# Kernel optimization log

Measured on AMD Instinct MI355X. Metric: run time of the kernel, lower is better.

The kernel has to match this reference:

```python
import jax, jax.numpy as jnp
import numpy as np

PI = 3.141592653589793


def setup_inputs() -> dict:
    key = jax.random.key(0)
    k1, k2, k3, k4 = jax.random.split(key, 4)
    B, N, C, H, V = 4, 4096, 128, 8, 16
    inputs = jax.random.normal(k1, (B, N, C), dtype=jnp.float32)
    dist = jax.random.uniform(k2, (N, N), dtype=jnp.float32)
    r = jax.random.normal(k3, (H, 1, 1), dtype=jnp.float32)
    weight = jax.random.normal(k4, (H, C, V), dtype=jnp.float32)
    return {"inputs": inputs, "dist": dist, "r": r, "weight": weight, "locality": 64}


def reference(inputs, dist, r, weight, locality):
    # scaled_dist: (H, N, N) -- learnable bandwidth per head via tan/sin transform
    scaled = dist[None, :, :] * jnp.tan(0.25 * PI * (1.0 + jnp.sin(r)))
    # quantile-based local masking along last axis (linear interpolation,
    # matching tfp.stats.percentile with interpolation='linear')
    mask = jnp.percentile(scaled, float(locality), axis=-1, keepdims=True, method="linear")
    fmax = jnp.finfo(jnp.float32).max
    scaled = jnp.where(scaled <= mask, scaled, fmax)
    # softmax over key axis of -scaled_dist (masked entries -> -fmax -> ~0 weight)
    att = jax.nn.softmax(-scaled, axis=-1)  # (H, N, N)
    # per-head value projection: (B,N,C) x (H,C,V) -> (B,H,N,V)
    value = jnp.einsum("bnj,hjk->bhnk", inputs, weight)
    # attention aggregation: (H,N,N) x (B,H,N,V) -> (B,H,N,V)
    concat = jnp.einsum("hnj,bhjd->bhnd", att, value)
    B, H, N, V = concat.shape
    concat = concat.transpose(0, 2, 1, 3).reshape(B, N, H * V)  # (B, N, hid_dim)
    # tf.keras.activations.gelu defaults to exact (non-approximate) gelu
    return jax.nn.gelu(concat, approximate=False)
```

## Files before the change

### kernel.cpp

```cpp
#include <hip/hip_runtime.h>
#include <hip/hip_bf16.h>
#include <math.h>

#define NN 4096
#define NC 128
#define NH 8
#define NV 16
#define NB 4
#define BD 64

typedef _Float16 half8 __attribute__((ext_vector_type(8)));
typedef __fp16  fp16x2 __attribute__((ext_vector_type(2)));
typedef float floatx4 __attribute__((ext_vector_type(4)));

__device__ __forceinline__ int get_loc(const int* locp){
    int lr = locp[0];
    return (lr >= 0 && lr <= 100) ? lr : 64;
}
__device__ __forceinline__ float head_scale(const float* rr, int h){
    float ts = tanf(0.78539816339744831f * (1.0f + sinf(rr[h])));
    if (!(ts > 0.f)) ts = (ts == 0.f) ? 1e-20f : 1e20f;
    if (ts > 1e20f) ts = 1e20f;
    return ts;
}
__device__ __forceinline__ void lds_barrier(){
    __asm__ __volatile__("s_waitcnt lgkmcnt(0)\n\ts_barrier" ::: "memory");
}

__global__ __launch_bounds__(256) void k_rowstats(const float* __restrict__ dist,
                                                  const int* __restrict__ locp,
                                                  float* __restrict__ Kval,
                                                  float* __restrict__ xminp){
    __shared__ unsigned int hist[4][256];
    __shared__ float cand[1024];
    __shared__ unsigned int cnt, selb_s, basec_s, xminu;
    const int i = blockIdx.x, t = threadIdx.x;
    const int wv = t >> 6, lane = t & 63;
    const int loc = get_loc(locp);
    const unsigned int rank = (unsigned int)(((long long)loc * (NN - 1)) / 100) + 1u;

    float v[16];
    const float4* rp = (const float4*)(dist + (size_t)i * NN);
#pragma unroll
    for (int k = 0; k < 4; k++){
        float4 x4 = rp[k * 256 + t];
        v[4*k+0] = x4.x; v[4*k+1] = x4.y; v[4*k+2] = x4.z; v[4*k+3] = x4.w;
    }
    for (int k = t; k < 1024; k += 256) ((unsigned int*)hist)[k] = 0;
    if (t == 0){ cnt = 0; selb_s = 255u; basec_s = 0u; xminu = 0xFFFFFFFFu; }
    __syncthreads();

    float lmin = 1e30f;
#pragma unroll
    for (int u = 0; u < 16; u++){
        float x = v[u];
        lmin = fminf(lmin, x);
        int b = (int)(x * 256.0f); b = b < 0 ? 0 : (b > 255 ? 255 : b);
        atomicAdd(&hist[wv][b], 1u);
    }
#pragma unroll
    for (int off = 1; off < 64; off <<= 1) lmin = fminf(lmin, __shfl_xor(lmin, off));
    if (lane == 0) atomicMin(&xminu, __float_as_uint(lmin));
    __syncthreads();

    if (t < 64){
        unsigned int lp[4];
        unsigned int run = 0;
#pragma unroll
        for (int q = 0; q < 4; q++){
            int b = 4 * t + q;
            run += hist[0][b] + hist[1][b] + hist[2][b] + hist[3][b];
            lp[q] = run;
        }
        unsigned int incl = run;
#pragma unroll
        for (int d = 1; d < 64; d <<= 1){
            unsigned int y = __shfl_up(incl, d);
            if (t >= d) incl += y;
        }
        unsigned int excl = incl - run;
        if (excl < rank && rank <= incl){
#pragma unroll
            for (int q = 0; q < 4; q++){
                if (excl + lp[q] >= rank){
                    selb_s  = (unsigned int)(4 * t + q);
                    basec_s = excl + (q ? lp[q-1] : 0u);
                    break;
                }
            }
        }
    }
    __syncthreads();
    const unsigned int sb = selb_s;
    if (t == 0) Kval[i] = ((float)sb + 1.0f) * 0.00390625f;
#pragma unroll
    for (int u = 0; u < 16; u++){
        float x = v[u];
        int b = (int)(x * 256.0f); b = b < 0 ? 0 : (b > 255 ? 255 : b);
        if ((unsigned int)b == sb){
            unsigned int idx = atomicAdd(&cnt, 1u);
            if (idx < 1024u) cand[idx] = x;
        }
    }
    __syncthreads();
    const unsigned int n = cnt > 1024u ? 1024u : cnt;
    const unsigned int need = rank - basec_s;
    for (unsigned int c0 = t; c0 < n; c0 += 256){
        float x = cand[c0];
        unsigned int lt = 0, le = 0;
        for (unsigned int k2 = 0; k2 < n; k2++){
            float y = cand[k2];
            lt += (y < x); le += (y <= x);
        }
        if (lt < need && need <= le) Kval[i] = x;
    }
    if (t == 0) xminp[i] = __uint_as_float(xminu);
}

__global__ __launch_bounds__(256) void k_value(const float* __restrict__ in,
                                               const float* __restrict__ wgt,
                                               _Float16* __restrict__ val_t){
    __shared__ float insh[NC * 65];
    __shared__ float wsh[NC * NV];
    const int j0 = blockIdx.x * 16;
    const int h  = blockIdx.y;
    const int t  = threadIdx.x;

    for (int k = t; k < NC * NV; k += 256) wsh[k] = wgt[h * NC * NV + k];
#pragma unroll
    for (int k = 0; k < 32; k++){
        int idx = k * 256 + t;
        int p = idx >> 7, c = idx & 127;
        int b = p >> 4, jl = p & 15;
        insh[c * 65 + jl * 4 + b] = in[((size_t)b * NN + j0 + jl) * NC + c];
    }
    __syncthreads();

    const int r = t & 63, dq = t >> 6;
    const int jl = r >> 2, b = r & 3;
    float a0 = 0.f, a1 = 0.f, a2 = 0.f, a3 = 0.f;
#pragma unroll 8
    for (int c = 0; c < NC; c++){
        float x = insh[c * 65 + r];
        float4 w4 = *(const float4*)&wsh[c * NV + dq * 4];
        a0 = fmaf(x, w4.x, a0);
        a1 = fmaf(x, w4.y, a1);
        a2 = fmaf(x, w4.z, a2);
        a3 = fmaf(x, w4.w, a3);
    }
    const size_t base = ((size_t)(h * BD + b * NV + dq * 4)) * NN + j0 + jl;
    val_t[base         ] = (_Float16)a0;
    val_t[base + NN    ] = (_Float16)a1;
    val_t[base + 2 * NN] = (_Float16)a2;
    val_t[base + 3 * NN] = (_Float16)a3;
}

__global__ __launch_bounds__(256) void k_att(const float* __restrict__ dist,
                                             const float* __restrict__ rr,
                                             const _Float16* __restrict__ val_t,
                                             const float* __restrict__ Kvalp,
                                             const float* __restrict__ xminp,
                                             float* __restrict__ out){
    __shared__ alignas(16) _Float16 wtile[2][32 * 72];
    __shared__ alignas(16) _Float16 vtile[2][64 * 72];

    const int l   = blockIdx.x + (NN / 32) * blockIdx.y;
    const int xcd = l & 7;
    const int s   = l >> 3;
    const int i0  = (xcd * 16 + (s >> 3)) * 32;
    const int h   = s & 7;

    const int t = threadIdx.x;
    const int lane = t & 63, wv = t >> 6;
    const float ts  = head_scale(rr, h);
    const float ts2 = ts * 1.44269504088896f;

    const int il = t >> 3, jq = t & 7;
    const int vrow = t >> 3, vpart = t & 7;
    const float kvi  = Kvalp[i0 + il];
    const float txmi = ts2 * xminp[i0 + il];
    const float nts2 = -ts2;

    half8 ones;
#pragma unroll
    for (int u = 0; u < 8; u++) ones[u] = (_Float16)1.0f;

    const float* dp = dist + (size_t)(i0 + il) * NN + jq * 8;
    const _Float16* vp0 = val_t + (size_t)(h * BD + vrow) * NN + vpart * 8;
    const _Float16* vp1 = vp0 + (size_t)32 * NN;

    floatx4 acc0 = (floatx4){0.f,0.f,0.f,0.f};
    floatx4 acc1 = (floatx4){0.f,0.f,0.f,0.f};
    floatx4 accs = (floatx4){0.f,0.f,0.f,0.f};

    const int is16 = (wv & 1) * 16;
    const int bh   = (wv >> 1) * 32;
    const int aoff  = (is16 + (lane & 15)) * 72 + (lane >> 4) * 8;
    const int boff0 = (bh + (lane & 15)) * 72 + (lane >> 4) * 8;
    const int boff1 = boff0 + 16 * 72;
    const int voff0 = vrow * 72 + vpart * 8;
    const int voff1 = (vrow + 32) * 72 + vpart * 8;
    const int woff  = il * 72 + jq * 8;

    uint4  Av0, Av1, Bv0, Bv1;
    float4 Ad0, Ad1, Bd0, Bd1;

#define LOADSET(V0, V1, D0, D1) do{                                          \
        V0 = *(const uint4*)vp0;  vp0 += 64;                                 \
        V1 = *(const uint4*)vp1;  vp1 += 64;                                 \
        D0 = *(const float4*)dp;                                             \
        D1 = *(const float4*)(dp + 4);  dp += 64; }while(0)

#define STAGE(BUF, V0, V1, D0, D1) do{                                       \
        *(uint4*)&vtile[BUF][voff0] = V0;                                    \
        *(uint4*)&vtile[BUF][voff1] = V1;                                    \
        const float dd_[8] = {D0.x,D0.y,D0.z,D0.w,D1.x,D1.y,D1.z,D1.w};      \
        union { half8 h8; fp16x2 h2[4]; } uu_;                               \
        _Pragma("unroll")                                                    \
        for (int u_ = 0; u_ < 4; u_++){                                      \
            float a0_ = fmaf(nts2, dd_[2*u_  ], txmi);                       \
            float a1_ = fmaf(nts2, dd_[2*u_+1], txmi);                       \
            a0_ = (dd_[2*u_  ] <= kvi) ? a0_ : -20000.0f;                    \
            a1_ = (dd_[2*u_+1] <= kvi) ? a1_ : -20000.0f;                    \
            uu_.h2[u_] = __builtin_amdgcn_cvt_pkrtz(                         \
                __builtin_amdgcn_exp2f(a0_), __builtin_amdgcn_exp2f(a1_));   \
        }                                                                    \
        *(half8*)&wtile[BUF][woff] = uu_.h8; }while(0)

#define MFMA_T(BUF) do{                                                      \
        _Pragma("unroll")                                                    \
        for (int kc_ = 0; kc_ < 2; kc_++){                                   \
            half8 af = *(const half8*)&wtile[BUF][aoff  + kc_ * 32];         \
            half8 b0 = *(const half8*)&vtile[BUF][boff0 + kc_ * 32];         \
            half8 b1 = *(const half8*)&vtile[BUF][boff1 + kc_ * 32];         \
            acc0 = __builtin_amdgcn_mfma_f32_16x16x32_f16(af, b0, acc0, 0, 0, 0); \
            acc1 = __builtin_amdgcn_mfma_f32_16x16x32_f16(af, b1, acc1, 0, 0, 0); \
            accs = __builtin_amdgcn_mfma_f32_16x16x32_f16(af, ones, accs, 0, 0, 0); \
        } }while(0)

    LOADSET(Av0, Av1, Ad0, Ad1);
    LOADSET(Bv0, Bv1, Bd0, Bd1);
    STAGE(0, Av0, Av1, Ad0, Ad1);

    for (int jp = 0; jp < 31; jp++){
        LOADSET(Av0, Av1, Ad0, Ad1);
        lds_barrier();
        MFMA_T(0);
        STAGE(1, Bv0, Bv1, Bd0, Bd1);
        LOADSET(Bv0, Bv1, Bd0, Bd1);
        lds_barrier();
        MFMA_T(1);
        STAGE(0, Av0, Av1, Ad0, Ad1);
    }
    lds_barrier();
    MFMA_T(0);
    STAGE(1, Bv0, Bv1, Bd0, Bd1);
    lds_barrier();
    MFMA_T(1);

#undef LOADSET
#undef STAGE
#undef MFMA_T

    const int m0 = (lane >> 4) * 4;
    const int d  = lane & 15;
#pragma unroll
    for (int r4 = 0; r4 < 4; r4++){
        const int iloc = is16 + m0 + r4;
        const float inv_s = 1.0f / fmaxf(accs[r4], 1e-30f);
#pragma unroll
        for (int nt = 0; nt < 2; nt++){
            const int b = (wv >> 1) * 2 + nt;
            float c = acc0[r4], c1 = acc1[r4];
            float cc = (nt == 0 ? c : c1) * inv_s;
            float g = 0.5f * cc * (1.0f + erff(cc * 0.70710678118654752f));
            out[((size_t)b * NN + i0 + iloc) * (NH * NV) + h * NV + d] = g;
        }
    }
}

extern "C" void kernel_launch(void* const* d_in, const int* in_sizes, int n_in,
                              void* d_out, int out_size, void* d_ws, size_t ws_size,
                              hipStream_t stream) {
    const float* in   = (const float*)d_in[0];
    const float* dist = (const float*)d_in[1];
    const float* r    = (const float*)d_in[2];
    const float* wgt  = (const float*)d_in[3];
    const int*   loc  = (const int*)d_in[4];
    float* out = (float*)d_out;

    float* Kval = (float*)d_ws;
    float* xmin = Kval + NN;
    _Float16* val_t = (_Float16*)((char*)d_ws + 2 * (size_t)NN * sizeof(float));

    k_rowstats<<<NN, 256, 0, stream>>>(dist, loc, Kval, xmin);
    k_value<<<dim3(NN / 16, NH), 256, 0, stream>>>(in, wgt, val_t);
    k_att<<<dim3(NN / 32, NH), 256, 0, stream>>>(dist, r, val_t, Kval, xmin, out);
}
```

Before: 177.6 us.

## Compute attention weights in registers and rewrite value projection with split-fp16 MFMA

The attention kernel now gives each wave 16 query rows and computes the softmax weights directly into MFMA A-fragments in registers. This drops the shared-memory weight tile, and each block covers 64 rows against all four batches, so every staged value tile is reused by more rows. The value projection is rewritten as an MFMA GEMM that splits each fp32 input into fp16 hi and lo parts to keep accuracy, replacing the scalar FMA loop. The cost is more registers per thread and a grid of fewer, larger blocks, which may lower occupancy.

```diff
diff --git a/kernel.cpp b/kernel.cpp
--- a/kernel.cpp
+++ b/kernel.cpp
@@ -120,39 +120,70 @@
 __global__ __launch_bounds__(256) void k_value(const float* __restrict__ in,
                                                const float* __restrict__ wgt,
                                                _Float16* __restrict__ val_t){
-    __shared__ float insh[NC * 65];
-    __shared__ float wsh[NC * NV];
-    const int j0 = blockIdx.x * 16;
-    const int h  = blockIdx.y;
-    const int t  = threadIdx.x;
-
-    for (int k = t; k < NC * NV; k += 256) wsh[k] = wgt[h * NC * NV + k];
-#pragma unroll
-    for (int k = 0; k < 32; k++){
-        int idx = k * 256 + t;
-        int p = idx >> 7, c = idx & 127;
-        int b = p >> 4, jl = p & 15;
-        insh[c * 65 + jl * 4 + b] = in[((size_t)b * NN + j0 + jl) * NC + c];
-    }
-    __syncthreads();
-
-    const int r = t & 63, dq = t >> 6;
-    const int jl = r >> 2, b = r & 3;
-    float a0 = 0.f, a1 = 0.f, a2 = 0.f, a3 = 0.f;
-#pragma unroll 8
-    for (int c = 0; c < NC; c++){
-        float x = insh[c * 65 + r];
-        float4 w4 = *(const float4*)&wsh[c * NV + dq * 4];
-        a0 = fmaf(x, w4.x, a0);
-        a1 = fmaf(x, w4.y, a1);
-        a2 = fmaf(x, w4.z, a2);
-        a3 = fmaf(x, w4.w, a3);
-    }
-    const size_t base = ((size_t)(h * BD + b * NV + dq * 4)) * NN + j0 + jl;
-    val_t[base         ] = (_Float16)a0;
-    val_t[base + NN    ] = (_Float16)a1;
-    val_t[base + 2 * NN] = (_Float16)a2;
-    val_t[base + 3 * NN] = (_Float16)a3;
+    __shared__ _Float16 Wt[NH * NV * 136];
+    const int b  = blockIdx.y;
+    const int j0 = blockIdx.x * 32;
+    const int t  = threadIdx.x, lane = t & 63, wv = t >> 6;
+
+    for (int w = t; w < NH * NC * NV; w += 256){
+        int h = w >> 11, c = (w >> 4) & 127, v = w & 15;
+        Wt[(h * 16 + v) * 136 + c] = (_Float16)wgt[w];
+    }
+    __syncthreads();
+
+    const int kl = (lane >> 4) * 8;
+    half8 Bf[2][4];
+#pragma unroll
+    for (int nt = 0; nt < 2; nt++){
+        const int hv = wv * 32 + nt * 16 + (lane & 15);
+#pragma unroll
+        for (int kc = 0; kc < 4; kc++)
+            Bf[nt][kc] = *(const half8*)&Wt[hv * 136 + kc * 32 + kl];
+    }
+
+    floatx4 acc[2][2];
+#pragma unroll
+    for (int a = 0; a < 2; a++)
+#pragma unroll
+        for (int c = 0; c < 2; c++) acc[a][c] = (floatx4){0.f,0.f,0.f,0.f};
+
+    const float* ip = in + ((size_t)b * NN + j0 + (lane & 15)) * NC + kl;
+#pragma unroll
+    for (int jm = 0; jm < 2; jm++){
+        const float* ipm = ip + jm * 16 * NC;
+#pragma unroll
+        for (int kc = 0; kc < 4; kc++){
+            float4 x0 = *(const float4*)(ipm + kc * 32);
+            float4 x1 = *(const float4*)(ipm + kc * 32 + 4);
+            const float xs[8] = {x0.x,x0.y,x0.z,x0.w,x1.x,x1.y,x1.z,x1.w};
+            union { half8 h8; fp16x2 h2[4]; } hi, lo;
+#pragma unroll
+            for (int u = 0; u < 4; u++){
+                hi.h2[u] = __builtin_amdgcn_cvt_pkrtz(xs[2*u], xs[2*u+1]);
+                float r0 = xs[2*u]   - (float)hi.h2[u][0];
+                float r1 = xs[2*u+1] - (float)hi.h2[u][1];
+                lo.h2[u] = __builtin_amdgcn_cvt_pkrtz(r0, r1);
+            }
+#pragma unroll
+            for (int nt = 0; nt < 2; nt++){
+                acc[jm][nt] = __builtin_amdgcn_mfma_f32_16x16x32_f16(hi.h8, Bf[nt][kc], acc[jm][nt], 0, 0, 0);
+                acc[jm][nt] = __builtin_amdgcn_mfma_f32_16x16x32_f16(lo.h8, Bf[nt][kc], acc[jm][nt], 0, 0, 0);
+            }
+        }
+    }
+
+    const int jw = (lane >> 4) * 4;
+#pragma unroll
+    for (int jm = 0; jm < 2; jm++)
+#pragma unroll
+        for (int nt = 0; nt < 2; nt++){
+            const int hv  = wv * 32 + nt * 16 + (lane & 15);
+            const int row = (hv >> 4) * BD + b * NV + (hv & 15);
+            union { _Float16 h[4]; uint2 u; } o;
+#pragma unroll
+            for (int u = 0; u < 4; u++) o.h[u] = (_Float16)acc[jm][nt][u];
+            *(uint2*)&val_t[(size_t)row * NN + j0 + jm * 16 + jw] = o.u;
+        }
 }
 
 __global__ __launch_bounds__(256) void k_att(const float* __restrict__ dist,
@@ -161,120 +192,126 @@
                                              const float* __restrict__ Kvalp,
                                              const float* __restrict__ xminp,
                                              float* __restrict__ out){
-    __shared__ alignas(16) _Float16 wtile[2][32 * 72];
     __shared__ alignas(16) _Float16 vtile[2][64 * 72];
 
-    const int l   = blockIdx.x + (NN / 32) * blockIdx.y;
+    const int l   = blockIdx.x + (NN / 64) * blockIdx.y;
     const int xcd = l & 7;
     const int s   = l >> 3;
-    const int i0  = (xcd * 16 + (s >> 3)) * 32;
+    const int i0  = (xcd * 8 + (s >> 3)) * 64;
     const int h   = s & 7;
 
-    const int t = threadIdx.x;
-    const int lane = t & 63, wv = t >> 6;
-    const float ts  = head_scale(rr, h);
-    const float ts2 = ts * 1.44269504088896f;
-
-    const int il = t >> 3, jq = t & 7;
+    const int t = threadIdx.x, lane = t & 63, wv = t >> 6;
+    const float ts   = head_scale(rr, h);
+    const float ts2  = ts * 1.44269504088896f;
+    const float nts2 = -ts2;
+
+    const int irow = i0 + wv * 16 + (lane & 15);
+    const float kvi  = Kvalp[irow];
+    const float txmi = ts2 * xminp[irow];
+
     const int vrow = t >> 3, vpart = t & 7;
-    const float kvi  = Kvalp[i0 + il];
-    const float txmi = ts2 * xminp[i0 + il];
-    const float nts2 = -ts2;
-
-    half8 ones;
-#pragma unroll
-    for (int u = 0; u < 8; u++) ones[u] = (_Float16)1.0f;
-
-    const float* dp = dist + (size_t)(i0 + il) * NN + jq * 8;
     const _Float16* vp0 = val_t + (size_t)(h * BD + vrow) * NN + vpart * 8;
     const _Float16* vp1 = vp0 + (size_t)32 * NN;
-
-    floatx4 acc0 = (floatx4){0.f,0.f,0.f,0.f};
-    floatx4 acc1 = (floatx4){0.f,0.f,0.f,0.f};
-    floatx4 accs = (floatx4){0.f,0.f,0.f,0.f};
-
-    const int is16 = (wv & 1) * 16;
-    const int bh   = (wv >> 1) * 32;
-    const int aoff  = (is16 + (lane & 15)) * 72 + (lane >> 4) * 8;
-    const int boff0 = (bh + (lane & 15)) * 72 + (lane >> 4) * 8;
-    const int boff1 = boff0 + 16 * 72;
     const int voff0 = vrow * 72 + vpart * 8;
     const int voff1 = (vrow + 32) * 72 + vpart * 8;
-    const int woff  = il * 72 + jq * 8;
+
+    const int kl = (lane >> 4) * 8;
+    const float* dp = dist + (size_t)irow * NN + kl;
+
+    const int bbase = (lane & 15) * 72 + kl;
+
+    half8 ones;
+#pragma unroll
+    for (int u = 0; u < 8; u++) ones[u] = (_Float16)1.0f;
+
+    floatx4 acc[4];
+#pragma unroll
+    for (int nt = 0; nt < 4; nt++) acc[nt] = (floatx4){0.f,0.f,0.f,0.f};
+    floatx4 accs = (floatx4){0.f,0.f,0.f,0.f};
 
     uint4  Av0, Av1, Bv0, Bv1;
-    float4 Ad0, Ad1, Bd0, Bd1;
-
-#define LOADSET(V0, V1, D0, D1) do{                                          \
+    float4 Ad[4], Bd[4];
+    half8  WA[2], WB[2];
+
+#define LOADD(D) do{                                                         \
+        D[0] = *(const float4*)dp;        D[1] = *(const float4*)(dp + 4);   \
+        D[2] = *(const float4*)(dp + 32); D[3] = *(const float4*)(dp + 36);  \
+        dp += 64; }while(0)
+
+#define LOADV(V0, V1) do{                                                    \
         V0 = *(const uint4*)vp0;  vp0 += 64;                                 \
-        V1 = *(const uint4*)vp1;  vp1 += 64;                                 \
-        D0 = *(const float4*)dp;                                             \
-        D1 = *(const float4*)(dp + 4);  dp += 64; }while(0)
-
-#define STAGE(BUF, V0, V1, D0, D1) do{                                       \
+        V1 = *(const uint4*)vp1;  vp1 += 64; }while(0)
+
+#define STAGEV(BUF, V0, V1) do{                                              \
         *(uint4*)&vtile[BUF][voff0] = V0;                                    \
-        *(uint4*)&vtile[BUF][voff1] = V1;                                    \
-        const float dd_[8] = {D0.x,D0.y,D0.z,D0.w,D1.x,D1.y,D1.z,D1.w};      \
-        union { half8 h8; fp16x2 h2[4]; } uu_;                               \
-        _Pragma("unroll")                                                    \
-        for (int u_ = 0; u_ < 4; u_++){                                      \
-            float a0_ = fmaf(nts2, dd_[2*u_  ], txmi);                       \
-            float a1_ = fmaf(nts2, dd_[2*u_+1], txmi);                       \
-            a0_ = (dd_[2*u_  ] <= kvi) ? a0_ : -20000.0f;                    \
-            a1_ = (dd_[2*u_+1] <= kvi) ? a1_ : -20000.0f;                    \
-            uu_.h2[u_] = __builtin_amdgcn_cvt_pkrtz(                         \
-                __builtin_amdgcn_exp2f(a0_), __builtin_amdgcn_exp2f(a1_));   \
-        }                                                                    \
-        *(half8*)&wtile[BUF][woff] = uu_.h8; }while(0)
-
-#define MFMA_T(BUF) do{                                                      \
+        *(uint4*)&vtile[BUF][voff1] = V1; }while(0)
+
+#define WCOMP(W, D) do{                                                      \
         _Pragma("unroll")                                                    \
         for (int kc_ = 0; kc_ < 2; kc_++){                                   \
-            half8 af = *(const half8*)&wtile[BUF][aoff  + kc_ * 32];         \
-            half8 b0 = *(const half8*)&vtile[BUF][boff0 + kc_ * 32];         \
-            half8 b1 = *(const half8*)&vtile[BUF][boff1 + kc_ * 32];         \
-            acc0 = __builtin_amdgcn_mfma_f32_16x16x32_f16(af, b0, acc0, 0, 0, 0); \
-            acc1 = __builtin_amdgcn_mfma_f32_16x16x32_f16(af, b1, acc1, 0, 0, 0); \
-            accs = __builtin_amdgcn_mfma_f32_16x16x32_f16(af, ones, accs, 0, 0, 0); \
-        } }while(0)
-
-    LOADSET(Av0, Av1, Ad0, Ad1);
-    LOADSET(Bv0, Bv1, Bd0, Bd1);
-    STAGE(0, Av0, Av1, Ad0, Ad1);
+            const float dd_[8] = {D[2*kc_].x, D[2*kc_].y, D[2*kc_].z, D[2*kc_].w, \
+                                  D[2*kc_+1].x, D[2*kc_+1].y, D[2*kc_+1].z, D[2*kc_+1].w}; \
+            union { half8 h8; fp16x2 h2[4]; } uu_;                           \
+            _Pragma("unroll")                                                \
+            for (int u_ = 0; u_ < 4; u_++){                                  \
+                float a0_ = fmaf(nts2, dd_[2*u_  ], txmi);                   \
+                float a1_ = fmaf(nts2, dd_[2*u_+1], txmi);                   \
+                a0_ = (dd_[2*u_  ] <= kvi) ? a0_ : -20000.0f;                \
+                a1_ = (dd_[2*u_+1] <= kvi) ? a1_ : -20000.0f;                \
+                uu_.h2[u_] = __builtin_amdgcn_cvt_pkrtz(                     \
+                    __builtin_amdgcn_exp2f(a0_), __builtin_amdgcn_exp2f(a1_)); \
+            }                                                                \
+            W[kc_] = uu_.h8; }                                               \
+        }while(0)
+
+#define MFMA_T(BUF, W) do{                                                   \
+        _Pragma("unroll")                                                    \
+        for (int kc_ = 0; kc_ < 2; kc_++){                                   \
+            half8 af_ = W[kc_];                                              \
+            accs = __builtin_amdgcn_mfma_f32_16x16x32_f16(af_, ones, accs, 0, 0, 0); \
+            _Pragma("unroll")                                                \
+            for (int nt_ = 0; nt_ < 4; nt_++){                               \
+                half8 bv_ = *(const half8*)&vtile[BUF][bbase + nt_ * 16 * 72 + kc_ * 32]; \
+                acc[nt_] = __builtin_amdgcn_mfma_f32_16x16x32_f16(af_, bv_, acc[nt_], 0, 0, 0); \
+            } } }while(0)
+
+    LOADD(Ad); LOADV(Av0, Av1);
+    LOADD(Bd); LOADV(Bv0, Bv1);
+    STAGEV(0, Av0, Av1); WCOMP(WA, Ad);
 
     for (int jp = 0; jp < 31; jp++){
-        LOADSET(Av0, Av1, Ad0, Ad1);
+        LOADD(Ad); LOADV(Av0, Av1);
         lds_barrier();
-        MFMA_T(0);
-        STAGE(1, Bv0, Bv1, Bd0, Bd1);
-        LOADSET(Bv0, Bv1, Bd0, Bd1);
+        MFMA_T(0, WA);
+        STAGEV(1, Bv0, Bv1); WCOMP(WB, Bd);
+        LOADD(Bd); LOADV(Bv0, Bv1);
         lds_barrier();
-        MFMA_T(1);
-        STAGE(0, Av0, Av1, Ad0, Ad1);
+        MFMA_T(1, WB);
+        STAGEV(0, Av0, Av1); WCOMP(WA, Ad);
     }
     lds_barrier();
-    MFMA_T(0);
-    STAGE(1, Bv0, Bv1, Bd0, Bd1);
+    MFMA_T(0, WA);
+    STAGEV(1, Bv0, Bv1); WCOMP(WB, Bd);
     lds_barrier();
-    MFMA_T(1);
-
-#undef LOADSET
-#undef STAGE
+    MFMA_T(1, WB);
+
+#undef LOADD
+#undef LOADV
+#undef STAGEV
+#undef WCOMP
 #undef MFMA_T
 
     const int m0 = (lane >> 4) * 4;
     const int d  = lane & 15;
 #pragma unroll
     for (int r4 = 0; r4 < 4; r4++){
-        const int iloc = is16 + m0 + r4;
+        const int i = i0 + wv * 16 + m0 + r4;
         const float inv_s = 1.0f / fmaxf(accs[r4], 1e-30f);
 #pragma unroll
-        for (int nt = 0; nt < 2; nt++){
-            const int b = (wv >> 1) * 2 + nt;
-            float c = acc0[r4], c1 = acc1[r4];
-            float cc = (nt == 0 ? c : c1) * inv_s;
+        for (int nt = 0; nt < 4; nt++){
+            float cc = acc[nt][r4] * inv_s;
             float g = 0.5f * cc * (1.0f + erff(cc * 0.70710678118654752f));
-            out[((size_t)b * NN + i0 + iloc) * (NH * NV) + h * NV + d] = g;
+            out[((size_t)nt * NN + i) * (NH * NV) + h * NV + d] = g;
         }
     }
 }
@@ -294,6 +331,6 @@
     _Float16* val_t = (_Float16*)((char*)d_ws + 2 * (size_t)NN * sizeof(float));
 
     k_rowstats<<<NN, 256, 0, stream>>>(dist, loc, Kval, xmin);
-    k_value<<<dim3(NN / 16, NH), 256, 0, stream>>>(in, wgt, val_t);
-    k_att<<<dim3(NN / 32, NH), 256, 0, stream>>>(dist, r, val_t, Kval, xmin, out);
-}
+    k_value<<<dim3(NN / 32, NB), 256, 0, stream>>>(in, wgt, val_t);
+    k_att<<<dim3(NN / 64, NH), 256, 0, stream>>>(dist, r, val_t, Kval, xmin, out);
+}
```

New measurement: 184.4 us. 3.8% more time.

## Merge value projection into row-stats kernel and compute it with split-fp16 MFMA

Applied to the files above, without the earlier changes.

Removes the separate value-projection kernel and folds it into a single prep launch, with the first 512 blocks computing the projection and the rest computing the per-row quantile stats. The projection now uses 16x16x32 fp16 MFMA, splitting each input into hi and lo fp16 parts to keep near-fp32 accuracy, and loads weights straight from global memory into registers instead of staging through LDS. This saves one kernel launch and lets the two independent workloads share the GPU. In exchange the weights are rounded to fp16, the MFMA count doubles because of the hi/lo split, and the combined kernel carries the larger LDS footprint of the row-stats path in every block.

```diff
diff --git a/kernel.cpp b/kernel.cpp
--- a/kernel.cpp
+++ b/kernel.cpp
@@ -27,15 +27,85 @@
     __asm__ __volatile__("s_waitcnt lgkmcnt(0)\n\ts_barrier" ::: "memory");
 }
 
-__global__ __launch_bounds__(256) void k_rowstats(const float* __restrict__ dist,
-                                                  const int* __restrict__ locp,
-                                                  float* __restrict__ Kval,
-                                                  float* __restrict__ xminp){
+__global__ __launch_bounds__(256) void k_prep(const float* __restrict__ dist,
+                                              const int* __restrict__ locp,
+                                              const float* __restrict__ in,
+                                              const float* __restrict__ wgt,
+                                              float* __restrict__ Kval,
+                                              float* __restrict__ xminp,
+                                              _Float16* __restrict__ val_t){
     __shared__ unsigned int hist[4][256];
     __shared__ float cand[1024];
     __shared__ unsigned int cnt, selb_s, basec_s, xminu;
-    const int i = blockIdx.x, t = threadIdx.x;
-    const int wv = t >> 6, lane = t & 63;
+
+    const int t = threadIdx.x, lane = t & 63, wv = t >> 6;
+
+    if (blockIdx.x < 512){
+        const int idx = blockIdx.x;
+        const int b   = idx & 3;
+        const int j0  = (idx >> 2) * 32;
+        const int kl  = (lane >> 4) * 8;
+        const int v   = lane & 15;
+
+        half8 Bf[2][4];
+#pragma unroll
+        for (int nt = 0; nt < 2; nt++){
+            const int h = wv * 2 + nt;
+            const float* wp = wgt + ((size_t)h * NC + kl) * NV + v;
+#pragma unroll
+            for (int kc = 0; kc < 4; kc++)
+#pragma unroll
+                for (int u = 0; u < 8; u++)
+                    Bf[nt][kc][u] = (_Float16)wp[(kc * 32 + u) * NV];
+        }
+
+        floatx4 acc[2][2];
+#pragma unroll
+        for (int a = 0; a < 2; a++)
+#pragma unroll
+            for (int c = 0; c < 2; c++) acc[a][c] = (floatx4){0.f,0.f,0.f,0.f};
+
+        const float* ip = in + ((size_t)b * NN + j0 + v) * NC + kl;
+#pragma unroll
+        for (int jm = 0; jm < 2; jm++){
+            const float* ipm = ip + jm * 16 * NC;
+#pragma unroll
+            for (int kc = 0; kc < 4; kc++){
+                float4 x0 = *(const float4*)(ipm + kc * 32);
+                float4 x1 = *(const float4*)(ipm + kc * 32 + 4);
+                const float xs[8] = {x0.x,x0.y,x0.z,x0.w,x1.x,x1.y,x1.z,x1.w};
+                union { half8 h8; fp16x2 h2[4]; } hi, lo;
+#pragma unroll
+                for (int u = 0; u < 4; u++){
+                    hi.h2[u] = __builtin_amdgcn_cvt_pkrtz(xs[2*u], xs[2*u+1]);
+                    float r0 = xs[2*u]   - (float)hi.h2[u][0];
+                    float r1 = xs[2*u+1] - (float)hi.h2[u][1];
+                    lo.h2[u] = __builtin_amdgcn_cvt_pkrtz(r0, r1);
+                }
+#pragma unroll
+                for (int nt = 0; nt < 2; nt++){
+                    acc[jm][nt] = __builtin_amdgcn_mfma_f32_16x16x32_f16(hi.h8, Bf[nt][kc], acc[jm][nt], 0, 0, 0);
+                    acc[jm][nt] = __builtin_amdgcn_mfma_f32_16x16x32_f16(lo.h8, Bf[nt][kc], acc[jm][nt], 0, 0, 0);
+                }
+            }
+        }
+
+        const int jw = (lane >> 4) * 4;
+#pragma unroll
+        for (int jm = 0; jm < 2; jm++)
+#pragma unroll
+            for (int nt = 0; nt < 2; nt++){
+                const int h   = wv * 2 + nt;
+                const int row = h * BD + b * NV + v;
+                union { _Float16 hh[4]; uint2 u; } o;
+#pragma unroll
+                for (int u = 0; u < 4; u++) o.hh[u] = (_Float16)acc[jm][nt][u];
+                *(uint2*)&val_t[(size_t)row * NN + j0 + jm * 16 + jw] = o.u;
+            }
+        return;
+    }
+
+    const int i = blockIdx.x - 512;
     const int loc = get_loc(locp);
     const unsigned int rank = (unsigned int)(((long long)loc * (NN - 1)) / 100) + 1u;
 
@@ -115,44 +185,6 @@
         if (lt < need && need <= le) Kval[i] = x;
     }
     if (t == 0) xminp[i] = __uint_as_float(xminu);
-}
-
-__global__ __launch_bounds__(256) void k_value(const float* __restrict__ in,
-                                               const float* __restrict__ wgt,
-                                               _Float16* __restrict__ val_t){
-    __shared__ float insh[NC * 65];
-    __shared__ float wsh[NC * NV];
-    const int j0 = blockIdx.x * 16;
-    const int h  = blockIdx.y;
-    const int t  = threadIdx.x;
-
-    for (int k = t; k < NC * NV; k += 256) wsh[k] = wgt[h * NC * NV + k];
-#pragma unroll
-    for (int k = 0; k < 32; k++){
-        int idx = k * 256 + t;
-        int p = idx >> 7, c = idx & 127;
-        int b = p >> 4, jl = p & 15;
-        insh[c * 65 + jl * 4 + b] = in[((size_t)b * NN + j0 + jl) * NC + c];
-    }
-    __syncthreads();
-
-    const int r = t & 63, dq = t >> 6;
-    const int jl = r >> 2, b = r & 3;
-    float a0 = 0.f, a1 = 0.f, a2 = 0.f, a3 = 0.f;
-#pragma unroll 8
-    for (int c = 0; c < NC; c++){
-        float x = insh[c * 65 + r];
-        float4 w4 = *(const float4*)&wsh[c * NV + dq * 4];
-        a0 = fmaf(x, w4.x, a0);
-        a1 = fmaf(x, w4.y, a1);
-        a2 = fmaf(x, w4.z, a2);
-        a3 = fmaf(x, w4.w, a3);
-    }
-    const size_t base = ((size_t)(h * BD + b * NV + dq * 4)) * NN + j0 + jl;
-    val_t[base         ] = (_Float16)a0;
-    val_t[base + NN    ] = (_Float16)a1;
-    val_t[base + 2 * NN] = (_Float16)a2;
-    val_t[base + 3 * NN] = (_Float16)a3;
 }
 
 __global__ __launch_bounds__(256) void k_att(const float* __restrict__ dist,
@@ -293,7 +325,6 @@
     float* xmin = Kval + NN;
     _Float16* val_t = (_Float16*)((char*)d_ws + 2 * (size_t)NN * sizeof(float));
 
-    k_rowstats<<<NN, 256, 0, stream>>>(dist, loc, Kval, xmin);
-    k_value<<<dim3(NN / 16, NH), 256, 0, stream>>>(in, wgt, val_t);
+    k_prep<<<512 + NN, 256, 0, stream>>>(dist, loc, in, wgt, Kval, xmin, val_t);
     k_att<<<dim3(NN / 32, NH), 256, 0, stream>>>(dist, r, val_t, Kval, xmin, out);
 }
```

Measured after the change: 168.5 us. -5.1%, faster.
